# Optimization experiments

Measured on AMD Instinct MI355X. Metric: run time of the kernel, lower is better.

Reference implementation:

```python
import jax, jax.numpy as jnp
import numpy as np
import math

# Static module config (matches init_kwargs)
C = 1.0            # ball curvature parameter c
IN_C, OUT_C = 512, 512
K, PAD = 3, 1
T, B = 2048, 16
EPS = 1e-15
RC = math.sqrt(C)

def _beta(a, b):
    return math.exp(math.lgamma(a) + math.lgamma(b) - math.lgamma(a + b))

BETA_NI = _beta(IN_C / 2.0, 0.5)            # beta(n_i/2, 1/2)
BETA_N = _beta(IN_C * K / 2.0, 0.5)         # beta(n/2, 1/2)
BETA_RATIO = BETA_N / BETA_NI
PROJ_EPS = 4e-3                              # geoopt float32 projection eps


def logmap0(y):
    # y in Poincare ball -> tangent at origin
    yn = jnp.clip(jnp.linalg.norm(y, axis=-1, keepdims=True), EPS, None)
    arg = jnp.clip(RC * yn, None, 1.0 - 1e-7)
    return y * (jnp.arctanh(arg) / (RC * yn))


def expmap0(u):
    un = jnp.clip(jnp.linalg.norm(u, axis=-1, keepdims=True), EPS, None)
    return jnp.tanh(RC * un) * u / (RC * un)


def project(x):
    maxnorm = (1.0 - PROJ_EPS) / RC
    norm = jnp.clip(jnp.linalg.norm(x, axis=-1, keepdims=True), EPS, None)
    return x * jnp.where(norm > maxnorm, maxnorm / norm, 1.0)


def poincare_linear(x, w_g, w_unit, b):
    # unidirectional Poincare MLR (geoopt_plusplus)
    rcx = RC * x                                             # [T,B,K*Cin]
    cx2 = jnp.sum(rcx * rcx, axis=-1, keepdims=True)         # [T,B,1]
    drcr = 2.0 * RC * b                                      # [Cout]
    num = 2.0 * jnp.einsum('tbi,io->tbo', rcx, w_unit) * jnp.cosh(drcr) \
          - (1.0 + cx2) * jnp.sinh(drcr)
    y = (2.0 * w_g / RC) * jnp.arcsinh(num / jnp.clip(1.0 - cx2, EPS, None))
    y = jnp.sinh(RC * y) / RC
    denom = 1.0 + jnp.sqrt(1.0 + C * jnp.sum(y * y, axis=-1, keepdims=True))
    return project(y / denom)


def setup_inputs() -> dict:
    key = jax.random.key(0)
    k1, k2, k3 = jax.random.split(key, 3)
    # points strictly inside the unit ball: ||x|| < 0.7
    v = jax.random.normal(k1, (T, B, IN_C), dtype=jnp.float32)
    vn = jnp.linalg.norm(v, axis=-1, keepdims=True)
    x = v / (1.0 + vn) * 0.7
    std = (2.0 * IN_C * K * OUT_C) ** -0.5
    w = jax.random.normal(k2, (K * IN_C, OUT_C), dtype=jnp.float32) * std
    weight_g = jnp.clip(jnp.linalg.norm(w, axis=0), 1e-15, None)   # [Cout]
    weight_v = w / weight_g                                        # [K*Cin, Cout]
    bias = jnp.zeros((OUT_C,), dtype=jnp.float32)
    return {"x": x, "weight_g": weight_g, "weight_v": weight_v, "bias": bias}


def reference(x, weight_g, weight_v, bias):
    u = logmap0(x) * BETA_RATIO                 # tangent space, rescaled
    u = jnp.pad(u, ((PAD, PAD), (0, 0), (0, 0)))
    olen = u.shape[0] - K + 1
    # im2col over time: [olen, B, K*Cin]
    u = jnp.concatenate([u[k:k + olen] for k in range(K)], axis=-1)
    xh = expmap0(u)
    w_unit = weight_v / jnp.clip(jnp.linalg.norm(weight_v, axis=0), EPS, None)
    return poincare_linear(xh, weight_g, w_unit, bias)
```

## Files before the change

kernel.cpp:

```cpp
#include <hip/hip_runtime.h>
#include <cstdint>
#include <cmath>

typedef unsigned short u16;
typedef short bf16x8 __attribute__((ext_vector_type(8)));
typedef float f32x4 __attribute__((ext_vector_type(4)));

#define T_DIM 2048
#define B_DIM 16
#define CIN 512
#define COUT 512
#define KIN 1536
#define NROWS (T_DIM * B_DIM)
#define UROWS ((T_DIM + 2) * B_DIM)

#define NTILES 24

#define LOG2E 1.44269504088896f
#define LN2   0.69314718055995f

__device__ __forceinline__ float fast_exp2(float x) {
#if __has_builtin(__builtin_amdgcn_exp2f)
  return __builtin_amdgcn_exp2f(x);
#else
  return __builtin_exp2f(x);
#endif
}
__device__ __forceinline__ float fast_log2(float x) {
#if __has_builtin(__builtin_amdgcn_logf)
  return __builtin_amdgcn_logf(x);
#else
  return __builtin_log2f(x);
#endif
}
__device__ __forceinline__ float fast_rcp(float x) {
  return __builtin_amdgcn_rcpf(x);
}

__device__ __forceinline__ u16 f2bf(float f) {
  unsigned u = __builtin_bit_cast(unsigned, f);
  u = (u + 0x7FFFu + ((u >> 16) & 1u)) >> 16;
  return (u16)u;
}

typedef __attribute__((address_space(3))) unsigned int as3u32;
typedef __attribute__((address_space(1))) unsigned int as1u32;

__device__ __forceinline__ void gload16(const u16* g, const u16* lds) {
#if __has_builtin(__builtin_amdgcn_global_load_lds)
  __builtin_amdgcn_global_load_lds((as1u32*)(uintptr_t)g,
                                   (as3u32*)(unsigned)(uintptr_t)lds, 16, 0, 0);
#else
  unsigned lane = __lane_id();
  ((uint4*)lds)[lane] = *(const uint4*)g;
#endif
}

__global__ __launch_bounds__(256) void k_colnorm(const float* __restrict__ wv,
                                                 float* __restrict__ partial) {
  int o = blockIdx.x * 256 + threadIdx.x;
  int r0 = blockIdx.y * 64;
  float s = 0.f;
#pragma unroll 8
  for (int r = 0; r < 64; ++r) {
    float v = wv[(size_t)(r0 + r) * COUT + o];
    s += v * v;
  }
  partial[(size_t)blockIdx.y * COUT + o] = s;
}

__global__ __launch_bounds__(256) void k_fin(const float* __restrict__ partial,
                                             float* __restrict__ invn) {
  int o = blockIdx.x * 256 + threadIdx.x;
  float s = 0.f;
#pragma unroll
  for (int j = 0; j < KIN / 64; ++j) s += partial[(size_t)j * COUT + o];
  invn[o] = 1.f / fmaxf(sqrtf(s), 1e-15f);
}

__global__ void k_chsh(const float* __restrict__ bias, float* __restrict__ ch,
                       float* __restrict__ sh) {
  int o = blockIdx.x * blockDim.x + threadIdx.x;
  if (o < COUT) {
    float d = 2.f * bias[o];
    float e = fast_exp2(d * LOG2E);
    float ie = fast_rcp(e);
    ch[o] = 0.5f * (e + ie);
    sh[o] = 0.5f * (e - ie);
  }
}

__global__ void k_wt(const float* __restrict__ wv, const float* __restrict__ invn,
                     u16* __restrict__ wt) {
  __shared__ float tile[64][65];
  int i0 = blockIdx.x * 64;
  int o0 = blockIdx.y * 64;
  int tx = threadIdx.x & 63, ty = threadIdx.x >> 6;
  for (int r = ty; r < 64; r += 4)
    tile[r][tx] = wv[(size_t)(i0 + r) * COUT + o0 + tx];
  __syncthreads();
  for (int r = ty; r < 64; r += 4) {
    float inv = invn[o0 + r];
    wt[(size_t)(o0 + r) * KIN + i0 + tx] = f2bf(tile[tx][r] * inv);
  }
}

__global__ void k_logmap(const float* __restrict__ x, u16* __restrict__ U,
                         float* __restrict__ nsq, float beta_ratio) {
  int row = blockIdx.x;
  int t = row >> 4;
  int lane = threadIdx.x;
  uint4* urow = (uint4*)(U + (size_t)row * CIN);
  if (t == 0 || t == T_DIM + 1) {
    uint4 z; z.x = z.y = z.z = z.w = 0u;
    urow[lane] = z;
    if (lane == 0) nsq[row] = 0.f;
    return;
  }
  const float4* xr = (const float4*)(x + (size_t)(row - 16) * CIN);
  float4 a = xr[lane * 2];
  float4 b = xr[lane * 2 + 1];
  float s = a.x*a.x + a.y*a.y + a.z*a.z + a.w*a.w
          + b.x*b.x + b.y*b.y + b.z*b.z + b.w*b.w;
#pragma unroll
  for (int d = 1; d < 64; d <<= 1) s += __shfl_xor(s, d);
  float r = sqrtf(s);
  float yn = fmaxf(r, 1e-15f);
  float arg = fminf(yn, 1.0f - 1e-7f);
  float at = 0.5f * LN2 * fast_log2((1.f + arg) * fast_rcp(1.f - arg));
  float f = at / yn * beta_ratio;
  union { u16 h[8]; uint4 v; } pk;
  pk.h[0] = f2bf(a.x * f); pk.h[1] = f2bf(a.y * f);
  pk.h[2] = f2bf(a.z * f); pk.h[3] = f2bf(a.w * f);
  pk.h[4] = f2bf(b.x * f); pk.h[5] = f2bf(b.y * f);
  pk.h[6] = f2bf(b.z * f); pk.h[7] = f2bf(b.w * f);
  urow[lane] = pk.v;
  if (lane == 0) nsq[row] = s * f * f;
}

__global__ __launch_bounds__(512, 2) void k_gemm(const u16* __restrict__ U,
                                                 const u16* __restrict__ WT,
                                                 float* __restrict__ out) {
  __shared__ u16 lA[2][2][8192];
  __shared__ u16 lB[2][2][8192];
  int bid = blockIdx.x;
  int wgid = (bid & 7) * 32 + (bid >> 3);
  int bm = wgid >> 1, bn = wgid & 1;
  int tid = threadIdx.x;
  int lane = tid & 63;
  int wid = tid >> 6;
  int wr = wid >> 2, wc = wid & 3;
  int lr = lane & 15;
  int srow = tid >> 2;
  int sc = (tid & 3) ^ ((tid >> 3) & 3);
  int cSwz = ((lane >> 4) ^ ((lr >> 1) & 3)) << 3;

  f32x4 acc[8][4] = {};

  auto stgA = [&](int tt, int h) {
    int ks32 = tt * 2 + h;
    int seg = ks32 >> 4;
    int c0 = (ks32 & 15) << 5;
    const u16* g = U + (size_t)(bm * 256 + seg * 16 + srow) * 512 + c0 + sc * 8;
    const u16* d = &lA[tt & 1][h][wid * 512];
    gload16(g, d);
    gload16(g + (size_t)128 * 512, d + 4096);
  };
  auto stgB = [&](int tt, int h) {
    int ks32 = tt * 2 + h;
    const u16* g = WT + (size_t)(bn * 256 + srow) * KIN + ks32 * 32 + sc * 8;
    const u16* d = &lB[tt & 1][h][wid * 512];
    gload16(g, d);
    gload16(g + (size_t)128 * KIN, d + 4096);
  };

  stgA(0, 0); stgB(0, 0); stgA(0, 1); stgB(0, 1);
  stgB(1, 0); stgA(1, 0); stgB(1, 1);
  asm volatile("s_waitcnt vmcnt(6)" ::: "memory");
  asm volatile("s_barrier" ::: "memory");

  for (int t = 0; t < NTILES; ++t) {
    int b = t & 1;
    const u16* pA = &lA[b][0][(wr * 128 + lr) * 32 + cSwz];
    const u16* pB = &lB[b][0][(wc * 64 + lr) * 32 + cSwz];
    bf16x8 af[4], bf[4];

#pragma unroll
    for (int i = 0; i < 4; ++i) bf[i] = *(const bf16x8*)(pB + i * 512);
#pragma unroll
    for (int i = 0; i < 4; ++i) af[i] = *(const bf16x8*)(pA + i * 512);
    if (t + 1 < NTILES) stgA(t + 1, 1);
    asm volatile("s_barrier" ::: "memory");
    asm volatile("s_waitcnt lgkmcnt(0)" ::: "memory");
    __builtin_amdgcn_s_setprio(1);
#pragma unroll
    for (int mi = 0; mi < 4; ++mi)
#pragma unroll
      for (int ni = 0; ni < 4; ++ni)
        acc[mi][ni] = __builtin_amdgcn_mfma_f32_16x16x32_bf16(
            af[mi], bf[ni], acc[mi][ni], 0, 0, 0);
    __builtin_amdgcn_s_setprio(0);
    asm volatile("s_barrier" ::: "memory");

#pragma unroll
    for (int i = 0; i < 4; ++i) af[i] = *(const bf16x8*)(pA + 2048 + i * 512);
    if (t + 2 < NTILES) stgB(t + 2, 0);
    asm volatile("s_barrier" ::: "memory");
    asm volatile("s_waitcnt lgkmcnt(0)" ::: "memory");
    __builtin_amdgcn_s_setprio(1);
#pragma unroll
    for (int mi = 0; mi < 4; ++mi)
#pragma unroll
      for (int ni = 0; ni < 4; ++ni)
        acc[4 + mi][ni] = __builtin_amdgcn_mfma_f32_16x16x32_bf16(
            af[mi], bf[ni], acc[4 + mi][ni], 0, 0, 0);
    __builtin_amdgcn_s_setprio(0);
    asm volatile("s_barrier" ::: "memory");

#pragma unroll
    for (int i = 0; i < 4; ++i) bf[i] = *(const bf16x8*)(pB + 8192 + i * 512);
#pragma unroll
    for (int i = 0; i < 4; ++i) af[i] = *(const bf16x8*)(pA + 8192 + i * 512);
    if (t + 2 < NTILES) stgA(t + 2, 0);
    asm volatile("s_barrier" ::: "memory");
    asm volatile("s_waitcnt lgkmcnt(0)" ::: "memory");
    __builtin_amdgcn_s_setprio(1);
#pragma unroll
    for (int mi = 0; mi < 4; ++mi)
#pragma unroll
      for (int ni = 0; ni < 4; ++ni)
        acc[mi][ni] = __builtin_amdgcn_mfma_f32_16x16x32_bf16(
            af[mi], bf[ni], acc[mi][ni], 0, 0, 0);
    __builtin_amdgcn_s_setprio(0);
    asm volatile("s_barrier" ::: "memory");

#pragma unroll
    for (int i = 0; i < 4; ++i) af[i] = *(const bf16x8*)(pA + 8192 + 2048 + i * 512);
    if (t + 2 < NTILES) stgB(t + 2, 1);
    if (t < NTILES - 2) asm volatile("s_waitcnt vmcnt(6)" ::: "memory");
    else                asm volatile("s_waitcnt vmcnt(0)" ::: "memory");
    asm volatile("s_barrier" ::: "memory");
    asm volatile("s_waitcnt lgkmcnt(0)" ::: "memory");
    __builtin_amdgcn_s_setprio(1);
#pragma unroll
    for (int mi = 0; mi < 4; ++mi)
#pragma unroll
      for (int ni = 0; ni < 4; ++ni)
        acc[4 + mi][ni] = __builtin_amdgcn_mfma_f32_16x16x32_bf16(
            af[mi], bf[ni], acc[4 + mi][ni], 0, 0, 0);
    __builtin_amdgcn_s_setprio(0);
    asm volatile("s_barrier" ::: "memory");
  }

  int orow = bm * 256 + wr * 128 + ((lane >> 4) << 2);
  int ocol = bn * 256 + wc * 64 + lr;
#pragma unroll
  for (int mi = 0; mi < 8; ++mi)
#pragma unroll
    for (int ni = 0; ni < 4; ++ni)
#pragma unroll
      for (int j = 0; j < 4; ++j)
        out[(size_t)(orow + mi * 16 + j) * COUT + (ocol + ni * 16)] = acc[mi][ni][j];
}

__global__ __launch_bounds__(128) void k_epi(float* __restrict__ out,
                                             const float* __restrict__ nsq,
                                             const float* __restrict__ wg,
                                             const float* __restrict__ chv,
                                             const float* __restrict__ shv) {
  int m = blockIdx.x;
  int tid = threadIdx.x;
  int lane = tid & 63, wv_ = tid >> 6;
  float un2 = nsq[m] + nsq[m + 16] + nsq[m + 32];
  float un = sqrtf(un2);
  float unc = fmaxf(un, 1e-15f);
  float e2 = fast_exp2(unc * (2.f * LOG2E));
  float th = (e2 - 1.f) * fast_rcp(e2 + 1.f);
  float sxp = th * fast_rcp(unc);
  float cx2 = sxp * sxp * un2;
  float iden = fast_rcp(fmaxf(1.f - cx2, 1e-15f));

  float4 dv = ((const float4*)(out + (size_t)m * COUT))[tid];
  float4 gv = ((const float4*)wg)[tid];
  float4 cv = ((const float4*)chv)[tid];
  float4 sv = ((const float4*)shv)[tid];
  float dot[4] = {dv.x, dv.y, dv.z, dv.w};
  float gvr[4] = {gv.x, gv.y, gv.z, gv.w};
  float chr[4] = {cv.x, cv.y, cv.z, cv.w};
  float shr[4] = {sv.x, sv.y, sv.z, sv.w};
  float y[4];
  float opc = 1.f + cx2;
#pragma unroll
  for (int e = 0; e < 4; ++e) {
    float num = 2.f * (sxp * dot[e]) * chr[e] - opc * shr[e];
    float z = num * iden;
    float w = z + sqrtf(fmaf(z, z, 1.f));
    float l = fast_log2(w);
    float E = fast_exp2((2.f * gvr[e]) * l);
    y[e] = 0.5f * (E - fast_rcp(E));
  }
  float ssl = y[0]*y[0] + y[1]*y[1] + y[2]*y[2] + y[3]*y[3];
#pragma unroll
  for (int d = 1; d < 64; d <<= 1) ssl += __shfl_xor(ssl, d);
  __shared__ float red[2];
  if (lane == 0) red[wv_] = ssl;
  __syncthreads();
  float ss = red[0] + red[1];
  float denom = 1.f + sqrtf(1.f + ss);
  float idn = 1.f / denom;
  float nrm = fmaxf(sqrtf(ss) * idn, 1e-15f);
  float maxn = 1.0f - 4e-3f;
  float scale = (nrm > maxn) ? (maxn / nrm) : 1.f;
  scale *= idn;
  float4 ov;
  ov.x = y[0] * scale;
  ov.y = y[1] * scale;
  ov.z = y[2] * scale;
  ov.w = y[3] * scale;
  ((float4*)(out + (size_t)m * COUT))[tid] = ov;
}

extern "C" void kernel_launch(void* const* d_in, const int* in_sizes, int n_in,
                              void* d_out, int out_size, void* d_ws, size_t ws_size,
                              hipStream_t stream) {
  const float* x    = (const float*)d_in[0];
  const float* wg   = (const float*)d_in[1];
  const float* wv   = (const float*)d_in[2];
  const float* bias = (const float*)d_in[3];
  float* out = (float*)d_out;

  char* ws = (char*)d_ws;
  u16*   U    = (u16*)(ws);
  float* NSQ  = (float*)(ws + 33587200);
  u16*   WT   = (u16*)(ws + 33718400);
  float* INVN = (float*)(ws + 35291264);
  float* CH   = (float*)(ws + 35293312);
  float* SH   = (float*)(ws + 35295360);
  float* PART = (float*)(ws + 35297408);

  double lb = (lgamma(768.0) + lgamma(0.5) - lgamma(768.5))
            - (lgamma(256.0) + lgamma(0.5) - lgamma(256.5));
  float beta_ratio = (float)exp(lb);

  k_colnorm<<<dim3(COUT / 256, KIN / 64), 256, 0, stream>>>(wv, PART);
  k_fin<<<COUT / 256, 256, 0, stream>>>(PART, INVN);
  k_chsh<<<COUT / 128, 128, 0, stream>>>(bias, CH, SH);
  k_wt<<<dim3(KIN / 64, COUT / 64), 256, 0, stream>>>(wv, INVN, WT);
  k_logmap<<<UROWS, 64, 0, stream>>>(x, U, NSQ, beta_ratio);
  k_gemm<<<(NROWS / 256) * (COUT / 256), 512, 0, stream>>>(U, WT, out);
  k_epi<<<NROWS, 128, 0, stream>>>(out, NSQ, wg, CH, SH);
}
```

Measured before the change: 118.1 us.

## Double-buffer LDS fragment registers in GEMM and fold cosh/sinh into k_fin

The GEMM main loop now preloads the next sub-step's A/B fragments into separate register sets before issuing the current MFMAs, and drops the explicit lgkmcnt(0) waits so LDS reads overlap matrix math. The first fragments of the next tile are loaded at the end of each iteration. Separately, the tiny cosh/sinh bias kernel is merged into the column-norm finalize kernel, which saves one launch. The change raises register pressure, and correctness depends on the compiler inserting proper waits for the LDS loads across the inline-asm barriers.

```diff
diff --git a/kernel.cpp b/kernel.cpp
--- a/kernel.cpp
+++ b/kernel.cpp
@@ -70,24 +70,20 @@
 }
 
 __global__ __launch_bounds__(256) void k_fin(const float* __restrict__ partial,
-                                             float* __restrict__ invn) {
+                                             const float* __restrict__ bias,
+                                             float* __restrict__ invn,
+                                             float* __restrict__ ch,
+                                             float* __restrict__ sh) {
   int o = blockIdx.x * 256 + threadIdx.x;
   float s = 0.f;
 #pragma unroll
   for (int j = 0; j < KIN / 64; ++j) s += partial[(size_t)j * COUT + o];
   invn[o] = 1.f / fmaxf(sqrtf(s), 1e-15f);
-}
-
-__global__ void k_chsh(const float* __restrict__ bias, float* __restrict__ ch,
-                       float* __restrict__ sh) {
-  int o = blockIdx.x * blockDim.x + threadIdx.x;
-  if (o < COUT) {
-    float d = 2.f * bias[o];
-    float e = fast_exp2(d * LOG2E);
-    float ie = fast_rcp(e);
-    ch[o] = 0.5f * (e + ie);
-    sh[o] = 0.5f * (e - ie);
-  }
+  float d = 2.f * bias[o];
+  float e = fast_exp2(d * LOG2E);
+  float ie = fast_rcp(e);
+  ch[o] = 0.5f * (e + ie);
+  sh[o] = 0.5f * (e - ie);
 }
 
 __global__ void k_wt(const float* __restrict__ wv, const float* __restrict__ invn,
@@ -179,75 +175,85 @@
   asm volatile("s_waitcnt vmcnt(6)" ::: "memory");
   asm volatile("s_barrier" ::: "memory");
 
+  bf16x8 afA[4], afB[4], bfE[4], bfO[4];
+  {
+    const u16* pA0 = &lA[0][0][(wr * 128 + lr) * 32 + cSwz];
+    const u16* pB0 = &lB[0][0][(wc * 64 + lr) * 32 + cSwz];
+#pragma unroll
+    for (int i = 0; i < 4; ++i) afA[i] = *(const bf16x8*)(pA0 + i * 512);
+#pragma unroll
+    for (int i = 0; i < 4; ++i) bfE[i] = *(const bf16x8*)(pB0 + i * 512);
+  }
+
   for (int t = 0; t < NTILES; ++t) {
     int b = t & 1;
     const u16* pA = &lA[b][0][(wr * 128 + lr) * 32 + cSwz];
     const u16* pB = &lB[b][0][(wc * 64 + lr) * 32 + cSwz];
-    bf16x8 af[4], bf[4];
-
-#pragma unroll
-    for (int i = 0; i < 4; ++i) bf[i] = *(const bf16x8*)(pB + i * 512);
-#pragma unroll
-    for (int i = 0; i < 4; ++i) af[i] = *(const bf16x8*)(pA + i * 512);
+    const u16* pAn = &lA[b ^ 1][0][(wr * 128 + lr) * 32 + cSwz];
+    const u16* pBn = &lB[b ^ 1][0][(wc * 64 + lr) * 32 + cSwz];
+
+#pragma unroll
+    for (int i = 0; i < 4; ++i) afB[i] = *(const bf16x8*)(pA + 2048 + i * 512);
     if (t + 1 < NTILES) stgA(t + 1, 1);
     asm volatile("s_barrier" ::: "memory");
-    asm volatile("s_waitcnt lgkmcnt(0)" ::: "memory");
     __builtin_amdgcn_s_setprio(1);
 #pragma unroll
     for (int mi = 0; mi < 4; ++mi)
 #pragma unroll
       for (int ni = 0; ni < 4; ++ni)
         acc[mi][ni] = __builtin_amdgcn_mfma_f32_16x16x32_bf16(
-            af[mi], bf[ni], acc[mi][ni], 0, 0, 0);
+            afA[mi], bfE[ni], acc[mi][ni], 0, 0, 0);
     __builtin_amdgcn_s_setprio(0);
     asm volatile("s_barrier" ::: "memory");
 
 #pragma unroll
-    for (int i = 0; i < 4; ++i) af[i] = *(const bf16x8*)(pA + 2048 + i * 512);
+    for (int i = 0; i < 4; ++i) afA[i] = *(const bf16x8*)(pA + 8192 + i * 512);
+#pragma unroll
+    for (int i = 0; i < 4; ++i) bfO[i] = *(const bf16x8*)(pB + 8192 + i * 512);
     if (t + 2 < NTILES) stgB(t + 2, 0);
     asm volatile("s_barrier" ::: "memory");
-    asm volatile("s_waitcnt lgkmcnt(0)" ::: "memory");
     __builtin_amdgcn_s_setprio(1);
 #pragma unroll
     for (int mi = 0; mi < 4; ++mi)
 #pragma unroll
       for (int ni = 0; ni < 4; ++ni)
         acc[4 + mi][ni] = __builtin_amdgcn_mfma_f32_16x16x32_bf16(
-            af[mi], bf[ni], acc[4 + mi][ni], 0, 0, 0);
+            afB[mi], bfE[ni], acc[4 + mi][ni], 0, 0, 0);
     __builtin_amdgcn_s_setprio(0);
     asm volatile("s_barrier" ::: "memory");
 
 #pragma unroll
-    for (int i = 0; i < 4; ++i) bf[i] = *(const bf16x8*)(pB + 8192 + i * 512);
-#pragma unroll
-    for (int i = 0; i < 4; ++i) af[i] = *(const bf16x8*)(pA + 8192 + i * 512);
+    for (int i = 0; i < 4; ++i)
+      afB[i] = *(const bf16x8*)(pA + 8192 + 2048 + i * 512);
     if (t + 2 < NTILES) stgA(t + 2, 0);
     asm volatile("s_barrier" ::: "memory");
-    asm volatile("s_waitcnt lgkmcnt(0)" ::: "memory");
     __builtin_amdgcn_s_setprio(1);
 #pragma unroll
     for (int mi = 0; mi < 4; ++mi)
 #pragma unroll
       for (int ni = 0; ni < 4; ++ni)
         acc[mi][ni] = __builtin_amdgcn_mfma_f32_16x16x32_bf16(
-            af[mi], bf[ni], acc[mi][ni], 0, 0, 0);
+            afA[mi], bfO[ni], acc[mi][ni], 0, 0, 0);
     __builtin_amdgcn_s_setprio(0);
     asm volatile("s_barrier" ::: "memory");
 
-#pragma unroll
-    for (int i = 0; i < 4; ++i) af[i] = *(const bf16x8*)(pA + 8192 + 2048 + i * 512);
+    if (t + 1 < NTILES) {
+#pragma unroll
+      for (int i = 0; i < 4; ++i) afA[i] = *(const bf16x8*)(pAn + i * 512);
+#pragma unroll
+      for (int i = 0; i < 4; ++i) bfE[i] = *(const bf16x8*)(pBn + i * 512);
+    }
     if (t + 2 < NTILES) stgB(t + 2, 1);
     if (t < NTILES - 2) asm volatile("s_waitcnt vmcnt(6)" ::: "memory");
     else                asm volatile("s_waitcnt vmcnt(0)" ::: "memory");
     asm volatile("s_barrier" ::: "memory");
-    asm volatile("s_waitcnt lgkmcnt(0)" ::: "memory");
     __builtin_amdgcn_s_setprio(1);
 #pragma unroll
     for (int mi = 0; mi < 4; ++mi)
 #pragma unroll
       for (int ni = 0; ni < 4; ++ni)
         acc[4 + mi][ni] = __builtin_amdgcn_mfma_f32_16x16x32_bf16(
-            af[mi], bf[ni], acc[4 + mi][ni], 0, 0, 0);
+            afB[mi], bfO[ni], acc[4 + mi][ni], 0, 0, 0);
     __builtin_amdgcn_s_setprio(0);
     asm volatile("s_barrier" ::: "memory");
   }
@@ -343,8 +349,7 @@
   float beta_ratio = (float)exp(lb);
 
   k_colnorm<<<dim3(COUT / 256, KIN / 64), 256, 0, stream>>>(wv, PART);
-  k_fin<<<COUT / 256, 256, 0, stream>>>(PART, INVN);
-  k_chsh<<<COUT / 128, 128, 0, stream>>>(bias, CH, SH);
+  k_fin<<<COUT / 256, 256, 0, stream>>>(PART, bias, INVN, CH, SH);
   k_wt<<<dim3(KIN / 64, COUT / 64), 256, 0, stream>>>(wv, INVN, WT);
   k_logmap<<<UROWS, 64, 0, stream>>>(x, U, NSQ, beta_ratio);
   k_gemm<<<(NROWS / 256) * (COUT / 256), 512, 0, stream>>>(U, WT, out);
```

New measurement: 115.6 us. 1.02x faster.
